# Optimization experiments

Hardware: AMD Instinct MI355X
Metric: run time of the kernel (lower is better)

## Reference

```python
import jax, jax.numpy as jnp
import numpy as np
import math

B, S, D, H = 8, 1024, 1024, 16
HD = D // H
MAX_LEN = 1024

def setup_inputs() -> dict:
    key = jax.random.key(0)
    ks = jax.random.split(key, 16)
    s = 1.0 / math.sqrt(D)
    return {
        "query": jax.random.normal(ks[0], (B, S, D), jnp.float32),
        "key_in": jax.random.normal(ks[1], (B, S, D), jnp.float32),
        "value": jax.random.normal(ks[2], (B, S, D), jnp.float32),
        "mask": jax.random.randint(ks[3], (B, S, S), 0, 2, jnp.int32),
        "Wq": jax.random.normal(ks[4], (D, D), jnp.float32) * s,
        "bq": jnp.zeros((D,), jnp.float32),
        "Wk": jax.random.normal(ks[5], (D, D), jnp.float32) * s,
        "bk": jnp.zeros((D,), jnp.float32),
        "Wv": jax.random.normal(ks[6], (D, D), jnp.float32) * s,
        "bv": jnp.zeros((D,), jnp.float32),
        "Wo": jax.random.normal(ks[7], (D, D), jnp.float32) * s,
        "bo": jnp.zeros((D,), jnp.float32),
        "syn_scores": jax.random.normal(ks[8], (H, MAX_LEN, MAX_LEN), jnp.float32) * 0.02,
        "alpha_param": jax.random.normal(ks[9], (1,), jnp.float32),
    }

def reference(query, key_in, value, mask, Wq, bq, Wk, bk, Wv, bv, Wo, bo, syn_scores, alpha_param):
    b, s, d = query.shape
    # projections (torch Linear: x @ W.T + b), split heads -> [b,h,s,hd]
    q = (query @ Wq.T + bq).reshape(b, s, H, HD).transpose(0, 2, 1, 3)
    k = (key_in @ Wk.T + bk).reshape(b, s, H, HD).transpose(0, 2, 1, 3)
    v = (value @ Wv.T + bv).reshape(b, s, H, HD).transpose(0, 2, 1, 3)
    scores = jnp.einsum("bhqd,bhkd->bhqk", q, k) / jnp.sqrt(jnp.float32(HD))
    # synthesizer scores: slice (seq_len <= max_sent_len path; equal-len matches torch)
    syn = syn_scores[:, :s, :s]  # [h,s,s]
    alpha = jax.nn.sigmoid(alpha_param)[0]
    merged = scores * alpha + (1.0 - alpha) * syn[None]
    merged = jnp.where(mask[:, None] == 0, jnp.float32(-1e9), merged)
    attn = jax.nn.softmax(merged, axis=-1)  # dropout disabled (eval)
    out = jnp.einsum("bhqk,bhkd->bhqd", attn, v)
    out = out.transpose(0, 2, 1, 3).reshape(b, s, d)
    return out @ Wo.T + bo
```

## Files before the change

### kernel.cpp

```cpp
#include <hip/hip_runtime.h>
#include <stdint.h>

#define BB 8
#define SS 1024
#define DD 1024
#define HH 16
#define HDIM 64

typedef _Float16 half8 __attribute__((ext_vector_type(8)));
typedef _Float16 half4 __attribute__((ext_vector_type(4)));
typedef float   float4v __attribute__((ext_vector_type(4)));
typedef float   float8v __attribute__((ext_vector_type(8)));

#define AS1(p) ((__attribute__((address_space(1))) void*)(p))
#define AS3(p) ((__attribute__((address_space(3))) void*)(p))

#define LOG2E 1.4426950408889634f

#if __has_builtin(__builtin_amdgcn_exp2f)
#define EXP2(x) __builtin_amdgcn_exp2f(x)
#else
#define EXP2(x) __expf((x) * 0.6931471805599453f)
#endif

struct CvtArgs {
    const float* src[8];
    _Float16*    dst[8];
    long long    n[8];
    int          scaled[8];
    const float* alp;
};

__global__ __launch_bounds__(256) void cvt_f32_f16(CvtArgs a) {
    const int seg = blockIdx.y;
    const long long n = a.n[seg];
    float s = 1.0f;
    if (a.scaled[seg]) s = (1.0f - 1.0f / (1.0f + __expf(-a.alp[0]))) * LOG2E;
    const float* __restrict__ src = a.src[seg];
    _Float16* __restrict__ dst = a.dst[seg];
    const long long stride = (long long)gridDim.x * 2048;
    for (long long base = ((long long)blockIdx.x * 256 + threadIdx.x) * 8;
         base < n; base += stride) {
        float8v u = *(const float8v*)(src + base);
        half8 h;
#pragma unroll
        for (int i = 0; i < 8; ++i) h[i] = (_Float16)(u[i] * s);
        *(half8*)(dst + base) = h;
    }
}

__global__ __launch_bounds__(256) void pack_mask(const int* __restrict__ mask,
                                                 unsigned long long* __restrict__ bits) {
    long long gid = (long long)blockIdx.x * 256 + threadIdx.x;
    int m = mask[gid];
    unsigned long long bal = __ballot(m != 0);
    if ((threadIdx.x & 63) == 0) bits[gid >> 6] = bal;
}

__device__ __forceinline__ void gemm_core(
    const _Float16* __restrict__ A, const _Float16* __restrict__ W,
    int m0, int n0, int wave, int lane, int wm, int wn,
    _Float16* As0, _Float16* Bs0, _Float16* As1, _Float16* Bs1,
    float4v (&acc)[4][4])
{
    constexpr int K = 1024, BK = 64;

    auto stage = [&](_Float16* Asb, _Float16* Bsb, int kt) {
#pragma unroll
        for (int i = 0; i < 4; ++i) {
            int flat = ((wave * 4 + i) * 64 + lane) * 8;
            int r = flat >> 6, c = flat & 63;
            const _Float16* ga = A + (long long)(m0 + r) * K + kt + c;
            const _Float16* gb = W + (long long)(n0 + r) * K + kt + c;
            __builtin_amdgcn_global_load_lds(AS1(ga), AS3(Asb + flat), 16, 0, 0);
            __builtin_amdgcn_global_load_lds(AS1(gb), AS3(Bsb + flat), 16, 0, 0);
        }
    };

    auto compute = [&](const _Float16* Asb, const _Float16* Bsb) {
#pragma unroll
        for (int kk = 0; kk < BK; kk += 32) {
            half8 af[4], bf[4];
#pragma unroll
            for (int t = 0; t < 4; ++t) {
                af[t] = *(const half8*)&Asb[(wm * 64 + t * 16 + (lane & 15)) * BK + kk + (lane >> 4) * 8];
                bf[t] = *(const half8*)&Bsb[(wn * 64 + t * 16 + (lane & 15)) * BK + kk + (lane >> 4) * 8];
            }
#pragma unroll
            for (int mt = 0; mt < 4; ++mt)
#pragma unroll
                for (int nt = 0; nt < 4; ++nt)
                    acc[mt][nt] = __builtin_amdgcn_mfma_f32_16x16x32_f16(af[mt], bf[nt], acc[mt][nt], 0, 0, 0);
        }
    };

    stage(As0, Bs0, 0);
    __syncthreads();
    for (int kt = 0; kt < K; kt += 2 * BK) {
        stage(As1, Bs1, kt + BK);
        compute(As0, Bs0);
        __syncthreads();
        if (kt + 2 * BK < K) stage(As0, Bs0, kt + 2 * BK);
        compute(As1, Bs1);
        __syncthreads();
    }
}

struct QkvArgs {
    const _Float16* A[3];
    const _Float16* W[3];
    const float*    bias[3];
    _Float16*       out[3];
    int             mode[3];
    const float*    alp;
};

__global__ __launch_bounds__(256) void gemm_qkv(QkvArgs g) {
    constexpr int BM = 128, BK = 64;
    __shared__ _Float16 As0[BM * BK], Bs0[BM * BK];
    __shared__ _Float16 As1[BM * BK], Bs1[BM * BK];

    const int z = blockIdx.z;
    const int tid  = threadIdx.x;
    const int lane = tid & 63;
    const int wave = tid >> 6;
    const int wm = wave >> 1, wn = wave & 1;
    const int m0 = blockIdx.x * BM;
    const int n0 = blockIdx.y * BM;

    float4v acc[4][4] = {};
    gemm_core(g.A[z], g.W[z], m0, n0, wave, lane, wm, wn, As0, Bs0, As1, Bs1, acc);

    const int mode = g.mode[z];
    float qscale = 1.0f;
    if (mode == 0) qscale = 0.125f * LOG2E / (1.0f + __expf(-g.alp[0]));
    _Float16* o = g.out[z];
    const float* bias = g.bias[z];

#pragma unroll
    for (int mt = 0; mt < 4; ++mt) {
#pragma unroll
        for (int nt = 0; nt < 4; ++nt) {
            int n  = n0 + wn * 64 + nt * 16 + (lane & 15);
            int mb = m0 + wm * 64 + mt * 16 + (lane >> 4) * 4;
            float bn = bias[n];
            int b = mb >> 10, sI = mb & 1023, hI = n >> 6, hd = n & 63;
            if (mode == 0) {
                long long idx = ((long long)(b * 16 + hI) * 1024 + sI) * 64 + hd;
#pragma unroll
                for (int i = 0; i < 4; ++i)
                    o[idx + (long long)i * 64] = (_Float16)((acc[mt][nt][i] + bn) * qscale);
            } else if (mode == 1) {
                long long tbase = (((long long)(b * 16 + hI)) * 16 + (sI >> 6)) * 4096;
#pragma unroll
                for (int i = 0; i < 4; ++i) {
                    int key = (sI & 63) + i;
                    o[tbase + (((key * 128 + hd * 2) ^ ((key & 7) << 4)) >> 1)] =
                        (_Float16)(acc[mt][nt][i] + bn);
                }
            } else {
                long long tbase = (((long long)(b * 16 + hI)) * 16 + (sI >> 6)) * 4096;
                int off = ((hd * 128 + (sI & 63) * 2) ^ ((hd & 15) << 3)) >> 1;
                half4 hv;
#pragma unroll
                for (int i = 0; i < 4; ++i) hv[i] = (_Float16)(acc[mt][nt][i] + bn);
                *(half4*)&o[tbase + off] = hv;
            }
        }
    }
}

__global__ __launch_bounds__(256) void gemm_o(
    const _Float16* __restrict__ A,
    const _Float16* __restrict__ W,
    const float* __restrict__ bias,
    float* __restrict__ out)
{
    constexpr int BM = 128, BK = 64;
    __shared__ _Float16 As0[BM * BK], Bs0[BM * BK];
    __shared__ _Float16 As1[BM * BK], Bs1[BM * BK];

    const int tid  = threadIdx.x;
    const int lane = tid & 63;
    const int wave = tid >> 6;
    const int wm = wave >> 1, wn = wave & 1;
    const int m0 = blockIdx.x * BM;
    const int n0 = blockIdx.y * BM;

    float4v acc[4][4] = {};
    gemm_core(A, W, m0, n0, wave, lane, wm, wn, As0, Bs0, As1, Bs1, acc);

#pragma unroll
    for (int mt = 0; mt < 4; ++mt) {
#pragma unroll
        for (int nt = 0; nt < 4; ++nt) {
            int n  = n0 + wn * 64 + nt * 16 + (lane & 15);
            int mb = m0 + wm * 64 + mt * 16 + (lane >> 4) * 4;
            float bn = bias[n];
#pragma unroll
            for (int i = 0; i < 4; ++i)
                out[(long long)(mb + i) * 1024 + n] = acc[mt][nt][i] + bn;
        }
    }
}

__global__ __launch_bounds__(256) void attn_kernel(
    const _Float16* __restrict__ qw,
    const _Float16* __restrict__ ktl,
    const _Float16* __restrict__ vtl,
    const unsigned long long* __restrict__ mbits,
    const _Float16* __restrict__ synh,
    _Float16* __restrict__ ao)
{
    __shared__ __align__(16) _Float16 KsA[4096];
    __shared__ __align__(16) _Float16 VsA[4096];
    __shared__ __align__(16) _Float16 KsB[4096];
    __shared__ __align__(16) _Float16 VsB[4096];

    const int tid  = threadIdx.x;
    const int lane = tid & 63;
    const int wave = tid >> 6;
    const int bid  = ((blockIdx.x & 7) << 7) | (blockIdx.x >> 3);
    const int b  = bid >> 7;
    const int h  = (bid >> 3) & 15;
    const int q0 = (bid & 7) * 128 + wave * 32;
    const int bh = b * 16 + h;

    half8 qf[2][2];
#pragma unroll
    for (int f = 0; f < 2; ++f) {
        const _Float16* qb = qw + ((long long)bh * SS + q0 + f * 16 + (lane & 15)) * HDIM + (lane >> 4) * 8;
        qf[f][0] = *(const half8*)qb;
        qf[f][1] = *(const half8*)(qb + 32);
    }

    float4v o[2][4] = {};
    float4v ol[2]   = {};
    float mrun[2] = {-3e38f, -3e38f};

    const _Float16* kgb = ktl + (long long)bh * 16 * 4096;
    const _Float16* vgb = vtl + (long long)bh * 16 * 4096;
    const unsigned long long* mb0 = mbits + ((long long)b * SS + q0 + (lane & 15)) * 16;
    const _Float16* syn0 = synh + ((long long)h * SS + q0 + (lane & 15)) * SS + ((lane >> 4) << 2);
    const _Float16* syn1 = syn0 + 16 * (long long)SS;

    const int tid8 = tid * 8;

    const int kswz = (lane & 7) << 4;
    const int kb0h = (((((lane & 15) << 7) + ((lane >> 4) << 4))      ) ^ kswz) >> 1;
    const int kb1h = (((((lane & 15) << 7) + ((lane >> 4) << 4)) + 64 ) ^ kswz) >> 1;
    int vbh[4];
#pragma unroll
    for (int ks = 0; ks < 4; ++ks)
        vbh[ks] = ((((lane & 15) << 7) + ks * 32 + ((lane >> 4) << 3)) ^ ((lane & 15) << 3)) >> 1;

    auto stage = [&](_Float16* Ksb, _Float16* Vsb, int t) {
        const _Float16* kg = kgb + t * 4096 + tid8;
        const _Float16* vg = vgb + t * 4096 + tid8;
        __builtin_amdgcn_global_load_lds(AS1(kg),        AS3(Ksb + tid8),        16, 0, 0);
        __builtin_amdgcn_global_load_lds(AS1(kg + 2048), AS3(Ksb + tid8 + 2048), 16, 0, 0);
        __builtin_amdgcn_global_load_lds(AS1(vg),        AS3(Vsb + tid8),        16, 0, 0);
        __builtin_amdgcn_global_load_lds(AS1(vg + 2048), AS3(Vsb + tid8 + 2048), 16, 0, 0);
    };

    half4 svA[2][4], svB[2][4];
    unsigned long long btA[2], btB[2];

    auto loadSyn = [&](int t, half4 (&sv)[2][4], unsigned long long (&bt)[2]) {
        bt[0] = mb0[t];
        bt[1] = mb0[256 + t];
        const int kb = t << 6;
#pragma unroll
        for (int ks = 0; ks < 4; ++ks) {
            sv[0][ks] = *(const half4*)(syn0 + kb + ks * 16);
            sv[1][ks] = *(const half4*)(syn1 + kb + ks * 16);
        }
    };

    const half4 vone = {(_Float16)1.f, (_Float16)1.f, (_Float16)1.f, (_Float16)1.f};

    auto compute = [&](const _Float16 (&Ks)[4096], const _Float16 (&Vs)[4096],
                       half4 (&sv)[2][4], unsigned long long (&bt)[2]) {
        float4v st[2][4];
#pragma unroll
        for (int ks = 0; ks < 4; ++ks) {
            half8 k0 = *(const half8*)&Ks[kb0h + ks * 1024];
            half8 k1 = *(const half8*)&Ks[kb1h + ks * 1024];
#pragma unroll
            for (int f = 0; f < 2; ++f) {
                float4v s;
#pragma unroll
                for (int i = 0; i < 4; ++i) s[i] = (float)sv[f][ks][i];
                s = __builtin_amdgcn_mfma_f32_16x16x32_f16(k0, qf[f][0], s, 0, 0, 0);
                s = __builtin_amdgcn_mfma_f32_16x16x32_f16(k1, qf[f][1], s, 0, 0, 0);
                st[f][ks] = s;
            }
        }
        half4 pf[2][4];
#pragma unroll
        for (int f = 0; f < 2; ++f) {
            const unsigned long long bits = bt[f];
            float tmax = -3e38f;
#pragma unroll
            for (int ks = 0; ks < 4; ++ks)
#pragma unroll
                for (int i = 0; i < 4; ++i) {
                    int pos = ks * 16 + ((lane >> 4) << 2) + i;
                    float sc = ((bits >> pos) & 1ull) ? st[f][ks][i] : -1e9f;
                    st[f][ks][i] = sc;
                    tmax = fmaxf(tmax, sc);
                }
            tmax = fmaxf(tmax, __shfl_xor(tmax, 16));
            tmax = fmaxf(tmax, __shfl_xor(tmax, 32));
            if (__any(tmax > mrun[f] + 8.0f)) {
                float mnew = fmaxf(mrun[f], tmax);
                float corr = EXP2(mrun[f] - mnew);
                float cr[4];
#pragma unroll
                for (int i = 0; i < 4; ++i) cr[i] = __shfl(corr, ((lane >> 4) << 2) + i);
#pragma unroll
                for (int n = 0; n < 4; ++n)
#pragma unroll
                    for (int i = 0; i < 4; ++i) o[f][n][i] *= cr[i];
#pragma unroll
                for (int i = 0; i < 4; ++i) ol[f][i] *= cr[i];
                mrun[f] = mnew;
            }
#pragma unroll
            for (int ks = 0; ks < 4; ++ks)
#pragma unroll
                for (int i = 0; i < 4; ++i)
                    pf[f][ks][i] = (_Float16)EXP2(st[f][ks][i] - mrun[f]);
        }
#pragma unroll
        for (int ks = 0; ks < 4; ++ks) {
            ol[0] = __builtin_amdgcn_mfma_f32_16x16x16f16(pf[0][ks], vone, ol[0], 0, 0, 0);
            ol[1] = __builtin_amdgcn_mfma_f32_16x16x16f16(pf[1][ks], vone, ol[1], 0, 0, 0);
#pragma unroll
            for (int n = 0; n < 4; ++n) {
                half4 vf = *(const half4*)&Vs[vbh[ks] + n * 1024];
                o[0][n] = __builtin_amdgcn_mfma_f32_16x16x16f16(pf[0][ks], vf, o[0][n], 0, 0, 0);
                o[1][n] = __builtin_amdgcn_mfma_f32_16x16x16f16(pf[1][ks], vf, o[1][n], 0, 0, 0);
            }
        }
    };

    stage(KsA, VsA, 0);
    loadSyn(0, svA, btA);
    __syncthreads();

    for (int t = 0; t < 16; t += 2) {
        stage(KsB, VsB, t + 1);
        loadSyn(t + 1, svB, btB);
        compute(KsA, VsA, svA, btA);
        __syncthreads();
        if (t + 2 < 16) {
            stage(KsA, VsA, t + 2);
            loadSyn(t + 2, svA, btA);
        }
        compute(KsB, VsB, svB, btB);
        __syncthreads();
    }

#pragma unroll
    for (int f = 0; f < 2; ++f) {
        float inv[4];
#pragma unroll
        for (int i = 0; i < 4; ++i) inv[i] = 1.0f / ol[f][i];
#pragma unroll
        for (int n = 0; n < 4; ++n)
#pragma unroll
            for (int i = 0; i < 4; ++i) {
                int qrow = q0 + f * 16 + (lane >> 4) * 4 + i;
                long long idx = ((long long)b * SS + qrow) * DD + h * 64 + n * 16 + (lane & 15);
                ao[idx] = (_Float16)(o[f][n][i] * inv[i]);
            }
    }
}

extern "C" void kernel_launch(void* const* d_in, const int* in_sizes, int n_in,
                              void* d_out, int out_size, void* d_ws, size_t ws_size,
                              hipStream_t stream) {
    const float* query  = (const float*)d_in[0];
    const float* key_in = (const float*)d_in[1];
    const float* value  = (const float*)d_in[2];
    const int*   mask   = (const int*)d_in[3];
    const float* Wq = (const float*)d_in[4];
    const float* bq = (const float*)d_in[5];
    const float* Wk = (const float*)d_in[6];
    const float* bk = (const float*)d_in[7];
    const float* Wv = (const float*)d_in[8];
    const float* bv = (const float*)d_in[9];
    const float* Wo = (const float*)d_in[10];
    const float* bo = (const float*)d_in[11];
    const float* syn = (const float*)d_in[12];
    const float* alp = (const float*)d_in[13];

    const long long XN = (long long)BB * SS * DD;
    const long long WN = (long long)DD * DD;
    const long long SN = (long long)HH * SS * SS;

    _Float16* ws = (_Float16*)d_ws;
    dim3 blk(256);
    dim3 ggrid(64, 8);

    if (ws_size >= ((size_t)140 << 20)) {
        _Float16* qx   = ws;
        _Float16* kx   = qx + XN;
        _Float16* vx   = kx + XN;
        _Float16* wqf  = vx + XN;
        _Float16* wkf  = wqf + WN;
        _Float16* wvf  = wkf + WN;
        _Float16* wof  = wvf + WN;
        _Float16* qws  = wof + WN;
        _Float16* kws  = qws + XN;
        _Float16* vTws = kws + XN;
        _Float16* synh = vTws + XN;
        unsigned long long* mbits = (unsigned long long*)(synh + SN);
        _Float16* ao = qx;

        CvtArgs a = {};
        a.src[0] = query;  a.dst[0] = qx;   a.n[0] = XN; a.scaled[0] = 0;
        a.src[1] = key_in; a.dst[1] = kx;   a.n[1] = XN; a.scaled[1] = 0;
        a.src[2] = value;  a.dst[2] = vx;   a.n[2] = XN; a.scaled[2] = 0;
        a.src[3] = Wq;     a.dst[3] = wqf;  a.n[3] = WN; a.scaled[3] = 0;
        a.src[4] = Wk;     a.dst[4] = wkf;  a.n[4] = WN; a.scaled[4] = 0;
        a.src[5] = Wv;     a.dst[5] = wvf;  a.n[5] = WN; a.scaled[5] = 0;
        a.src[6] = Wo;     a.dst[6] = wof;  a.n[6] = WN; a.scaled[6] = 0;
        a.src[7] = syn;    a.dst[7] = synh; a.n[7] = SN; a.scaled[7] = 1;
        a.alp = alp;
        cvt_f32_f16<<<dim3(2048, 8), blk, 0, stream>>>(a);

        pack_mask<<<dim3(32768), blk, 0, stream>>>(mask, mbits);

        QkvArgs g;
        g.A[0] = qx;  g.W[0] = wqf; g.bias[0] = bq; g.out[0] = qws;  g.mode[0] = 0;
        g.A[1] = kx;  g.W[1] = wkf; g.bias[1] = bk; g.out[1] = kws;  g.mode[1] = 1;
        g.A[2] = vx;  g.W[2] = wvf; g.bias[2] = bv; g.out[2] = vTws; g.mode[2] = 2;
        g.alp = alp;
        gemm_qkv<<<dim3(64, 8, 3), blk, 0, stream>>>(g);

        attn_kernel<<<dim3(1024), blk, 0, stream>>>(qws, kws, vTws, mbits, synh, ao);

        gemm_o<<<ggrid, blk, 0, stream>>>(ao, wof, bo, (float*)d_out);
    } else {
        _Float16* xbuf = ws;
        _Float16* wqf  = ws + XN;
        _Float16* wkf  = wqf + WN;
        _Float16* wvf  = wkf + WN;
        _Float16* wof  = wvf + WN;
        _Float16* qws  = wof + WN;
        _Float16* kws  = qws + XN;
        _Float16* vTws = kws + XN;
        _Float16* synh = vTws + XN;
        unsigned long long* mbits = (unsigned long long*)(synh + SN);
        _Float16* ao = xbuf;

        CvtArgs a1 = {};
        a1.src[0] = query; a1.dst[0] = xbuf; a1.n[0] = XN; a1.scaled[0] = 0;
        a1.src[1] = Wq;    a1.dst[1] = wqf;  a1.n[1] = WN; a1.scaled[1] = 0;
        a1.src[2] = Wk;    a1.dst[2] = wkf;  a1.n[2] = WN; a1.scaled[2] = 0;
        a1.src[3] = Wv;    a1.dst[3] = wvf;  a1.n[3] = WN; a1.scaled[3] = 0;
        a1.src[4] = Wo;    a1.dst[4] = wof;  a1.n[4] = WN; a1.scaled[4] = 0;
        a1.src[5] = syn;   a1.dst[5] = synh; a1.n[5] = SN; a1.scaled[5] = 1;
        a1.alp = alp;
        cvt_f32_f16<<<dim3(2048, 6), blk, 0, stream>>>(a1);

        pack_mask<<<dim3(32768), blk, 0, stream>>>(mask, mbits);

        QkvArgs g;
        g.alp = alp;
        g.A[0] = xbuf; g.W[0] = wqf; g.bias[0] = bq; g.out[0] = qws; g.mode[0] = 0;
        gemm_qkv<<<dim3(64, 8, 1), blk, 0, stream>>>(g);

        CvtArgs a2 = a1; a2.src[0] = key_in;
        cvt_f32_f16<<<dim3(2048, 1), blk, 0, stream>>>(a2);
        g.A[0] = xbuf; g.W[0] = wkf; g.bias[0] = bk; g.out[0] = kws; g.mode[0] = 1;
        gemm_qkv<<<dim3(64, 8, 1), blk, 0, stream>>>(g);

        CvtArgs a3 = a1; a3.src[0] = value;
        cvt_f32_f16<<<dim3(2048, 1), blk, 0, stream>>>(a3);
        g.A[0] = xbuf; g.W[0] = wvf; g.bias[0] = bv; g.out[0] = vTws; g.mode[0] = 2;
        gemm_qkv<<<dim3(64, 8, 1), blk, 0, stream>>>(g);

        attn_kernel<<<dim3(1024), blk, 0, stream>>>(qws, kws, vTws, mbits, synh, ao);

        gemm_o<<<ggrid, blk, 0, stream>>>(ao, wof, bo, (float*)d_out);
    }
}
```

Measured before the change: 465.7 us.

## Fuse fp32-to-fp16 activation conversion into QKV GEMM and swizzle tile order

```diff
diff --git a/kernel.cpp b/kernel.cpp
--- a/kernel.cpp
+++ b/kernel.cpp
@@ -57,57 +57,29 @@
     if ((threadIdx.x & 63) == 0) bits[gid >> 6] = bal;
 }
 
-__device__ __forceinline__ void gemm_core(
-    const _Float16* __restrict__ A, const _Float16* __restrict__ W,
-    int m0, int n0, int wave, int lane, int wm, int wn,
-    _Float16* As0, _Float16* Bs0, _Float16* As1, _Float16* Bs1,
-    float4v (&acc)[4][4])
+__device__ __forceinline__ void gemm_tile_compute(
+    const _Float16* __restrict__ Asb, const _Float16* __restrict__ Bsb,
+    int lane, int wm, int wn, float4v (&acc)[4][4])
 {
-    constexpr int K = 1024, BK = 64;
-
-    auto stage = [&](_Float16* Asb, _Float16* Bsb, int kt) {
-#pragma unroll
-        for (int i = 0; i < 4; ++i) {
-            int flat = ((wave * 4 + i) * 64 + lane) * 8;
-            int r = flat >> 6, c = flat & 63;
-            const _Float16* ga = A + (long long)(m0 + r) * K + kt + c;
-            const _Float16* gb = W + (long long)(n0 + r) * K + kt + c;
-            __builtin_amdgcn_global_load_lds(AS1(ga), AS3(Asb + flat), 16, 0, 0);
-            __builtin_amdgcn_global_load_lds(AS1(gb), AS3(Bsb + flat), 16, 0, 0);
-        }
-    };
-
-    auto compute = [&](const _Float16* Asb, const _Float16* Bsb) {
-#pragma unroll
-        for (int kk = 0; kk < BK; kk += 32) {
-            half8 af[4], bf[4];
-#pragma unroll
-            for (int t = 0; t < 4; ++t) {
-                af[t] = *(const half8*)&Asb[(wm * 64 + t * 16 + (lane & 15)) * BK + kk + (lane >> 4) * 8];
-                bf[t] = *(const half8*)&Bsb[(wn * 64 + t * 16 + (lane & 15)) * BK + kk + (lane >> 4) * 8];
-            }
-#pragma unroll
-            for (int mt = 0; mt < 4; ++mt)
-#pragma unroll
-                for (int nt = 0; nt < 4; ++nt)
-                    acc[mt][nt] = __builtin_amdgcn_mfma_f32_16x16x32_f16(af[mt], bf[nt], acc[mt][nt], 0, 0, 0);
-        }
-    };
-
-    stage(As0, Bs0, 0);
-    __syncthreads();
-    for (int kt = 0; kt < K; kt += 2 * BK) {
-        stage(As1, Bs1, kt + BK);
-        compute(As0, Bs0);
-        __syncthreads();
-        if (kt + 2 * BK < K) stage(As0, Bs0, kt + 2 * BK);
-        compute(As1, Bs1);
-        __syncthreads();
+    constexpr int BK = 64;
+#pragma unroll
+    for (int kk = 0; kk < BK; kk += 32) {
+        half8 af[4], bf[4];
+#pragma unroll
+        for (int t = 0; t < 4; ++t) {
+            af[t] = *(const half8*)&Asb[(wm * 64 + t * 16 + (lane & 15)) * BK + kk + (lane >> 4) * 8];
+            bf[t] = *(const half8*)&Bsb[(wn * 64 + t * 16 + (lane & 15)) * BK + kk + (lane >> 4) * 8];
+        }
+#pragma unroll
+        for (int mt = 0; mt < 4; ++mt)
+#pragma unroll
+            for (int nt = 0; nt < 4; ++nt)
+                acc[mt][nt] = __builtin_amdgcn_mfma_f32_16x16x32_f16(af[mt], bf[nt], acc[mt][nt], 0, 0, 0);
     }
 }
 
 struct QkvArgs {
-    const _Float16* A[3];
+    const float*    A[3];
     const _Float16* W[3];
     const float*    bias[3];
     _Float16*       out[3];
@@ -116,7 +88,7 @@
 };
 
 __global__ __launch_bounds__(256) void gemm_qkv(QkvArgs g) {
-    constexpr int BM = 128, BK = 64;
+    constexpr int BM = 128, BK = 64, K = 1024;
     __shared__ _Float16 As0[BM * BK], Bs0[BM * BK];
     __shared__ _Float16 As1[BM * BK], Bs1[BM * BK];
 
@@ -125,11 +97,63 @@
     const int lane = tid & 63;
     const int wave = tid >> 6;
     const int wm = wave >> 1, wn = wave & 1;
-    const int m0 = blockIdx.x * BM;
-    const int n0 = blockIdx.y * BM;
+    const int id = blockIdx.x;
+    const int xt = ((id & 7) << 3) | ((id >> 3) & 7);
+    const int yt = id >> 6;
+    const int m0 = xt * BM;
+    const int n0 = yt * BM;
+
+    const float*    __restrict__ A = g.A[z];
+    const _Float16* __restrict__ W = g.W[z];
 
     float4v acc[4][4] = {};
-    gemm_core(g.A[z], g.W[z], m0, n0, wave, lane, wm, wn, As0, Bs0, As1, Bs1, acc);
+
+    auto loadA = [&](float8v (&ar)[4], int kt) {
+#pragma unroll
+        for (int i = 0; i < 4; ++i) {
+            int flat = ((wave * 4 + i) * 64 + lane) * 8;
+            int r = flat >> 6, c = flat & 63;
+            ar[i] = *(const float8v*)(A + (long long)(m0 + r) * K + kt + c);
+        }
+    };
+    auto writeA = [&](_Float16* Asb, float8v (&ar)[4]) {
+#pragma unroll
+        for (int i = 0; i < 4; ++i) {
+            int flat = ((wave * 4 + i) * 64 + lane) * 8;
+            half8 h;
+#pragma unroll
+            for (int j = 0; j < 8; ++j) h[j] = (_Float16)ar[i][j];
+            *(half8*)&Asb[flat] = h;
+        }
+    };
+    auto stageW = [&](_Float16* Bsb, int kt) {
+#pragma unroll
+        for (int i = 0; i < 4; ++i) {
+            int flat = ((wave * 4 + i) * 64 + lane) * 8;
+            int r = flat >> 6, c = flat & 63;
+            __builtin_amdgcn_global_load_lds(AS1(W + (long long)(n0 + r) * K + kt + c),
+                                             AS3(Bsb + flat), 16, 0, 0);
+        }
+    };
+
+    float8v arA[4], arB[4];
+    loadA(arA, 0);
+    stageW(Bs0, 0);
+    writeA(As0, arA);
+    __syncthreads();
+
+    for (int kt = 0; kt < K; kt += 2 * BK) {
+        loadA(arB, kt + BK);
+        stageW(Bs1, kt + BK);
+        gemm_tile_compute(As0, Bs0, lane, wm, wn, acc);
+        writeA(As1, arB);
+        __syncthreads();
+        const bool more = (kt + 2 * BK) < K;
+        if (more) { loadA(arA, kt + 2 * BK); stageW(Bs0, kt + 2 * BK); }
+        gemm_tile_compute(As1, Bs1, lane, wm, wn, acc);
+        if (more) writeA(As0, arA);
+        __syncthreads();
+    }
 
     const int mode = g.mode[z];
     float qscale = 1.0f;
@@ -176,7 +200,7 @@
     const float* __restrict__ bias,
     float* __restrict__ out)
 {
-    constexpr int BM = 128, BK = 64;
+    constexpr int BM = 128, BK = 64, K = 1024;
     __shared__ _Float16 As0[BM * BK], Bs0[BM * BK];
     __shared__ _Float16 As1[BM * BK], Bs1[BM * BK];
 
@@ -184,11 +208,36 @@
     const int lane = tid & 63;
     const int wave = tid >> 6;
     const int wm = wave >> 1, wn = wave & 1;
-    const int m0 = blockIdx.x * BM;
-    const int n0 = blockIdx.y * BM;
+    const int id = blockIdx.x;
+    const int xt = ((id & 7) << 3) | ((id >> 3) & 7);
+    const int yt = id >> 6;
+    const int m0 = xt * BM;
+    const int n0 = yt * BM;
 
     float4v acc[4][4] = {};
-    gemm_core(A, W, m0, n0, wave, lane, wm, wn, As0, Bs0, As1, Bs1, acc);
+
+    auto stage = [&](_Float16* Asb, _Float16* Bsb, int kt) {
+#pragma unroll
+        for (int i = 0; i < 4; ++i) {
+            int flat = ((wave * 4 + i) * 64 + lane) * 8;
+            int r = flat >> 6, c = flat & 63;
+            __builtin_amdgcn_global_load_lds(AS1(A + (long long)(m0 + r) * K + kt + c),
+                                             AS3(Asb + flat), 16, 0, 0);
+            __builtin_amdgcn_global_load_lds(AS1(W + (long long)(n0 + r) * K + kt + c),
+                                             AS3(Bsb + flat), 16, 0, 0);
+        }
+    };
+
+    stage(As0, Bs0, 0);
+    __syncthreads();
+    for (int kt = 0; kt < K; kt += 2 * BK) {
+        stage(As1, Bs1, kt + BK);
+        gemm_tile_compute(As0, Bs0, lane, wm, wn, acc);
+        __syncthreads();
+        if (kt + 2 * BK < K) stage(As0, Bs0, kt + 2 * BK);
+        gemm_tile_compute(As1, Bs1, lane, wm, wn, acc);
+        __syncthreads();
+    }
 
 #pragma unroll
     for (int mt = 0; mt < 4; ++mt) {
@@ -400,91 +449,39 @@
     const long long WN = (long long)DD * DD;
     const long long SN = (long long)HH * SS * SS;
 
-    _Float16* ws = (_Float16*)d_ws;
+    _Float16* ws   = (_Float16*)d_ws;
+    _Float16* wqf  = ws;
+    _Float16* wkf  = wqf + WN;
+    _Float16* wvf  = wkf + WN;
+    _Float16* wof  = wvf + WN;
+    _Float16* qws  = wof + WN;
+    _Float16* kws  = qws + XN;
+    _Float16* vTws = kws + XN;
+    _Float16* synh = vTws + XN;
+    _Float16* ao   = synh + SN;
+    unsigned long long* mbits = (unsigned long long*)(ao + XN);
+
     dim3 blk(256);
-    dim3 ggrid(64, 8);
-
-    if (ws_size >= ((size_t)140 << 20)) {
-        _Float16* qx   = ws;
-        _Float16* kx   = qx + XN;
-        _Float16* vx   = kx + XN;
-        _Float16* wqf  = vx + XN;
-        _Float16* wkf  = wqf + WN;
-        _Float16* wvf  = wkf + WN;
-        _Float16* wof  = wvf + WN;
-        _Float16* qws  = wof + WN;
-        _Float16* kws  = qws + XN;
-        _Float16* vTws = kws + XN;
-        _Float16* synh = vTws + XN;
-        unsigned long long* mbits = (unsigned long long*)(synh + SN);
-        _Float16* ao = qx;
-
-        CvtArgs a = {};
-        a.src[0] = query;  a.dst[0] = qx;   a.n[0] = XN; a.scaled[0] = 0;
-        a.src[1] = key_in; a.dst[1] = kx;   a.n[1] = XN; a.scaled[1] = 0;
-        a.src[2] = value;  a.dst[2] = vx;   a.n[2] = XN; a.scaled[2] = 0;
-        a.src[3] = Wq;     a.dst[3] = wqf;  a.n[3] = WN; a.scaled[3] = 0;
-        a.src[4] = Wk;     a.dst[4] = wkf;  a.n[4] = WN; a.scaled[4] = 0;
-        a.src[5] = Wv;     a.dst[5] = wvf;  a.n[5] = WN; a.scaled[5] = 0;
-        a.src[6] = Wo;     a.dst[6] = wof;  a.n[6] = WN; a.scaled[6] = 0;
-        a.src[7] = syn;    a.dst[7] = synh; a.n[7] = SN; a.scaled[7] = 1;
-        a.alp = alp;
-        cvt_f32_f16<<<dim3(2048, 8), blk, 0, stream>>>(a);
-
-        pack_mask<<<dim3(32768), blk, 0, stream>>>(mask, mbits);
-
-        QkvArgs g;
-        g.A[0] = qx;  g.W[0] = wqf; g.bias[0] = bq; g.out[0] = qws;  g.mode[0] = 0;
-        g.A[1] = kx;  g.W[1] = wkf; g.bias[1] = bk; g.out[1] = kws;  g.mode[1] = 1;
-        g.A[2] = vx;  g.W[2] = wvf; g.bias[2] = bv; g.out[2] = vTws; g.mode[2] = 2;
-        g.alp = alp;
-        gemm_qkv<<<dim3(64, 8, 3), blk, 0, stream>>>(g);
-
-        attn_kernel<<<dim3(1024), blk, 0, stream>>>(qws, kws, vTws, mbits, synh, ao);
-
-        gemm_o<<<ggrid, blk, 0, stream>>>(ao, wof, bo, (float*)d_out);
-    } else {
-        _Float16* xbuf = ws;
-        _Float16* wqf  = ws + XN;
-        _Float16* wkf  = wqf + WN;
-        _Float16* wvf  = wkf + WN;
-        _Float16* wof  = wvf + WN;
-        _Float16* qws  = wof + WN;
-        _Float16* kws  = qws + XN;
-        _Float16* vTws = kws + XN;
-        _Float16* synh = vTws + XN;
-        unsigned long long* mbits = (unsigned long long*)(synh + SN);
-        _Float16* ao = xbuf;
-
-        CvtArgs a1 = {};
-        a1.src[0] = query; a1.dst[0] = xbuf; a1.n[0] = XN; a1.scaled[0] = 0;
-        a1.src[1] = Wq;    a1.dst[1] = wqf;  a1.n[1] = WN; a1.scaled[1] = 0;
-        a1.src[2] = Wk;    a1.dst[2] = wkf;  a1.n[2] = WN; a1.scaled[2] = 0;
-        a1.src[3] = Wv;    a1.dst[3] = wvf;  a1.n[3] = WN; a1.scaled[3] = 0;
-        a1.src[4] = Wo;    a1.dst[4] = wof;  a1.n[4] = WN; a1.scaled[4] = 0;
-        a1.src[5] = syn;   a1.dst[5] = synh; a1.n[5] = SN; a1.scaled[5] = 1;
-        a1.alp = alp;
-        cvt_f32_f16<<<dim3(2048, 6), blk, 0, stream>>>(a1);
-
-        pack_mask<<<dim3(32768), blk, 0, stream>>>(mask, mbits);
-
-        QkvArgs g;
-        g.alp = alp;
-        g.A[0] = xbuf; g.W[0] = wqf; g.bias[0] = bq; g.out[0] = qws; g.mode[0] = 0;
-        gemm_qkv<<<dim3(64, 8, 1), blk, 0, stream>>>(g);
-
-        CvtArgs a2 = a1; a2.src[0] = key_in;
-        cvt_f32_f16<<<dim3(2048, 1), blk, 0, stream>>>(a2);
-        g.A[0] = xbuf; g.W[0] = wkf; g.bias[0] = bk; g.out[0] = kws; g.mode[0] = 1;
-        gemm_qkv<<<dim3(64, 8, 1), blk, 0, stream>>>(g);
-
-        CvtArgs a3 = a1; a3.src[0] = value;
-        cvt_f32_f16<<<dim3(2048, 1), blk, 0, stream>>>(a3);
-        g.A[0] = xbuf; g.W[0] = wvf; g.bias[0] = bv; g.out[0] = vTws; g.mode[0] = 2;
-        gemm_qkv<<<dim3(64, 8, 1), blk, 0, stream>>>(g);
-
-        attn_kernel<<<dim3(1024), blk, 0, stream>>>(qws, kws, vTws, mbits, synh, ao);
-
-        gemm_o<<<ggrid, blk, 0, stream>>>(ao, wof, bo, (float*)d_out);
-    }
-}
+
+    CvtArgs a = {};
+    a.src[0] = Wq;  a.dst[0] = wqf;  a.n[0] = WN; a.scaled[0] = 0;
+    a.src[1] = Wk;  a.dst[1] = wkf;  a.n[1] = WN; a.scaled[1] = 0;
+    a.src[2] = Wv;  a.dst[2] = wvf;  a.n[2] = WN; a.scaled[2] = 0;
+    a.src[3] = Wo;  a.dst[3] = wof;  a.n[3] = WN; a.scaled[3] = 0;
+    a.src[4] = syn; a.dst[4] = synh; a.n[4] = SN; a.scaled[4] = 1;
+    a.alp = alp;
+    cvt_f32_f16<<<dim3(2048, 5), blk, 0, stream>>>(a);
+
+    pack_mask<<<dim3(32768), blk, 0, stream>>>(mask, mbits);
+
+    QkvArgs g;
+    g.A[0] = query;  g.W[0] = wqf; g.bias[0] = bq; g.out[0] = qws;  g.mode[0] = 0;
+    g.A[1] = key_in; g.W[1] = wkf; g.bias[1] = bk; g.out[1] = kws;  g.mode[1] = 1;
+    g.A[2] = value;  g.W[2] = wvf; g.bias[2] = bv; g.out[2] = vTws; g.mode[2] = 2;
+    g.alp = alp;
+    gemm_qkv<<<dim3(512, 1, 3), blk, 0, stream>>>(g);
+
+    attn_kernel<<<dim3(1024), blk, 0, stream>>>(qws, kws, vTws, mbits, synh, ao);
+
+    gemm_o<<<dim3(512), blk, 0, stream>>>(ao, wof, bo, (float*)d_out);
+}
```

Result: no change. 457.0 us (-1.9%).
